# Performance work log

Measured on AMD Instinct MI355X. Metric: run time of the kernel, lower is better.

The kernel has to match this reference:

```python
import jax, jax.numpy as jnp
import numpy as np

POOL = 7                     # cfg.POOLING_SIZE
PRE = 2 * POOL               # pre_pool_size (max_pool=True path)
LEVEL_HW = (256, 128, 64, 32)  # square H=W of P2..P5 for a 1024x1024 image


def setup_inputs() -> dict:
    key = jax.random.key(0)
    ks = jax.random.split(key, 8)
    C = 256
    feats = {f"p{i + 2}": jax.random.normal(ks[i], (1, C, s, s), dtype=jnp.float32)
             for i, s in enumerate(LEVEL_HW)}
    N = 1000
    IMG = 1024.0
    x1 = jax.random.uniform(ks[4], (N,), minval=0.0, maxval=IMG - 33.0)
    y1 = jax.random.uniform(ks[5], (N,), minval=0.0, maxval=IMG - 33.0)
    w = jax.random.uniform(ks[6], (N,), minval=32.0, maxval=512.0)
    h = jax.random.uniform(ks[7], (N,), minval=32.0, maxval=512.0)
    x2 = jnp.minimum(x1 + w, IMG - 1.0)
    y2 = jnp.minimum(y1 + h, IMG - 1.0)
    rois = jnp.stack([jnp.zeros((N,), jnp.float32), x1, y1, x2, y2], axis=1)
    inp = dict(feats)
    inp["rois"] = rois
    return inp


def _crop_pool_fpn(p2, p3, p4, p5, rois):
    """Faithful vectorized version of Network._crop_pool_layer_fpn (max_pool=True).

    Per-ROI FPN level select, affine-grid + bilinear grid_sample
    (align_corners=True semantics, zeros padding), then 2x2 max pool.
    """
    levels = (p2, p3, p4, p5)
    C = p2.shape[1]
    Hm = p2.shape[2]  # largest (P2) map; all levels padded up to this
    # Pad every level into one [L, Hm, Wm, C] array (NHWC for clean gathers).
    feats = jnp.stack([
        jnp.pad(jnp.transpose(f[0], (1, 2, 0)),
                ((0, Hm - f.shape[2]), (0, Hm - f.shape[3]), (0, 0)))
        for f in levels])

    x1, y1, x2, y2 = rois[:, 1], rois[:, 2], rois[:, 3], rois[:, 4]
    w = jnp.where(x2 - x1 <= 0, 1e-14, x2 - x1)
    h = jnp.where(y2 - y1 <= 0, 1e-14, y2 - y1)
    kf = 4.0 + jnp.log2(jnp.sqrt(w * h) / 224.0)   # k0 + log2(sqrt(wh)/224)
    kf = jnp.clip(kf, 2.0, 5.0)                     # clamp BEFORE round (as in source)
    k = jnp.round(kf)
    scale = 2.0 ** k
    lvl = k.astype(jnp.int32) - 2                   # [N] in [0,4)
    x1s, y1s, x2s, y2s = x1 / scale, y1 / scale, x2 / scale, y2 / scale

    # affine_grid(theta) + align_corners=True grid_sample collapses to direct
    # pixel coords: px = (x1+x2)/2 + t*(x2-x1)/2, t = linspace(-1, 1, PRE).
    t = jnp.linspace(-1.0, 1.0, PRE)
    px = (x1s + x2s)[:, None] * 0.5 + t[None, :] * ((x2s - x1s)[:, None] * 0.5)  # [N,PRE]
    py = (y1s + y2s)[:, None] * 0.5 + t[None, :] * ((y2s - y1s)[:, None] * 0.5)
    PX = jnp.broadcast_to(px[:, None, :], (px.shape[0], PRE, PRE))  # [N,PRE,PRE]
    PY = jnp.broadcast_to(py[:, :, None], (py.shape[0], PRE, PRE))

    HWl = jnp.asarray(LEVEL_HW, jnp.float32)[lvl][:, None, None]  # per-ROI level size (square)
    x0 = jnp.floor(PX)
    y0 = jnp.floor(PY)
    dx = PX - x0
    dy = PY - y0

    def gather(yi, xi):
        inb = ((xi >= 0) & (xi < HWl) & (yi >= 0) & (yi < HWl)).astype(feats.dtype)
        yc = jnp.clip(yi, 0, Hm - 1).astype(jnp.int32)
        xc = jnp.clip(xi, 0, Hm - 1).astype(jnp.int32)
        v = feats[lvl[:, None, None], yc, xc]      # [N,PRE,PRE,C]
        return v * inb[..., None]                   # zeros padding

    out = (gather(y0, x0) * ((1 - dy) * (1 - dx))[..., None]
           + gather(y0, x0 + 1) * ((1 - dy) * dx)[..., None]
           + gather(y0 + 1, x0) * (dy * (1 - dx))[..., None]
           + gather(y0 + 1, x0 + 1) * (dy * dx)[..., None])  # [N,PRE,PRE,C]

    crops = jnp.transpose(out, (0, 3, 1, 2))        # [N,C,PRE,PRE]
    N = crops.shape[0]
    crops = crops.reshape(N, C, POOL, 2, POOL, 2).max(axis=(3, 5))  # 2x2 max pool
    return crops                                     # [N,C,POOL,POOL]


def reference(p2, p3, p4, p5, rois):
    return _crop_pool_fpn(p2, p3, p4, p5, rois)
```

## Files before the change

kernel.cpp:

```cpp
#include <hip/hip_runtime.h>
#include <math.h>

#define C_CH 256
#define PRE 14
#define NPOOL 7
#define PIX (NPOOL * NPOOL)
#define OUT_PER_ROI (C_CH * PIX)
#define HALF_C 128
#define HALF_OUT (HALF_C * PIX)
#define SROW 132

#define OFF_P2 0
#define OFF_P3 16777216u
#define OFF_P4 20971520u
#define OFF_P5 22020096u
#define WS_ELEMS 22282240u

#define RB 528

static __device__ __forceinline__ unsigned short f2bf(float f) {
    unsigned int u = __float_as_uint(f);
    unsigned int r = (u + 0x7FFFu + ((u >> 16) & 1u)) >> 16;
    return (unsigned short)r;
}
static __device__ __forceinline__ float bf2f(unsigned short b) {
    return __uint_as_float(((unsigned int)b) << 16);
}

__global__ __launch_bounds__(256) void transpose_all_k(
    const float* __restrict__ p2, const float* __restrict__ p3,
    const float* __restrict__ p4, const float* __restrict__ p5,
    unsigned short* __restrict__ ws) {
    __shared__ unsigned char lds[128 * RB];

    int b = blockIdx.x;
    const float* __restrict__ src;
    int HW2; unsigned int off;
    if (b < 512)      { src = p2; HW2 = 65536; off = OFF_P2; }
    else if (b < 640) { src = p3; HW2 = 16384; off = OFF_P3; b -= 512; }
    else if (b < 672) { src = p4; HW2 = 4096;  off = OFF_P4; b -= 640; }
    else              { src = p5; HW2 = 1024;  off = OFF_P5; b -= 672; }
    const int hw0 = b << 7;

    const int t   = threadIdx.x;
    const int hwq = t & 31;
    const int cg  = t >> 5;

    const int key = (hwq & 7) << 4;

    #pragma unroll
    for (int s = 0; s < 8; ++s) {
        const int c0 = (cg << 2) + (s << 5);
        const float* g = src + (size_t)c0 * HW2 + hw0 + (hwq << 2);
        const float4 a0 = *(const float4*)(g);
        const float4 a1 = *(const float4*)(g + HW2);
        const float4 a2 = *(const float4*)(g + 2 * (size_t)HW2);
        const float4 a3 = *(const float4*)(g + 3 * (size_t)HW2);
        const int cb = (c0 << 1) ^ key;
        unsigned char* base = &lds[(hwq << 2) * RB + cb];
        ushort4 w;
        w.x = f2bf(a0.x); w.y = f2bf(a1.x); w.z = f2bf(a2.x); w.w = f2bf(a3.x);
        *(ushort4*)(base) = w;
        w.x = f2bf(a0.y); w.y = f2bf(a1.y); w.z = f2bf(a2.y); w.w = f2bf(a3.y);
        *(ushort4*)(base + RB) = w;
        w.x = f2bf(a0.z); w.y = f2bf(a1.z); w.z = f2bf(a2.z); w.w = f2bf(a3.z);
        *(ushort4*)(base + 2 * RB) = w;
        w.x = f2bf(a0.w); w.y = f2bf(a1.w); w.z = f2bf(a2.w); w.w = f2bf(a3.w);
        *(ushort4*)(base + 3 * RB) = w;
    }
    __syncthreads();

    char* __restrict__ dstb = (char*)(ws + off + ((size_t)hw0 << 8));
    const int chunk = t & 31;
    const int hwl   = t >> 5;
    #pragma unroll
    for (int p = 0; p < 16; ++p) {
        const int hw = (p << 3) + hwl;
        const int k2 = ((hw >> 2) & 7) << 4;
        const uint4 v = *(const uint4*)&lds[hw * RB + ((chunk << 4) ^ k2)];
        *(uint4*)(dstb + hw * 512 + (chunk << 4)) = v;
    }
}

template <bool HWC>
__global__ __launch_bounds__(256, 6) void roi_align_k(
    const float* __restrict__ p2, const float* __restrict__ p3,
    const float* __restrict__ p4, const float* __restrict__ p5,
    const unsigned short* __restrict__ ws, const float* __restrict__ rois,
    float* __restrict__ out) {

    __shared__ float sxw0[PRE], sxw1[PRE], syw0[PRE], syw1[PRE];
    __shared__ int   sxc0[PRE], sxc1[PRE], syc0[PRE], syc1[PRE];
    __shared__ float sout[PIX * SROW];

    const int n   = blockIdx.x;
    const int ch0 = blockIdx.y << 7;
    const float x1 = rois[n * 5 + 1];
    const float y1 = rois[n * 5 + 2];
    const float x2 = rois[n * 5 + 3];
    const float y2 = rois[n * 5 + 4];

    float w = x2 - x1; w = (w <= 0.f) ? 1e-14f : w;
    float h = y2 - y1; h = (h <= 0.f) ? 1e-14f : h;
    float kf = 4.f + log2f(sqrtf(w * h) * (1.f / 224.f));
    kf = fminf(fmaxf(kf, 2.f), 5.f);
    const float kr = rintf(kf);
    const int   lvl = (int)kr - 2;
    const float scale = exp2f(kr);
    const int   HW = 256 >> lvl;

    const int t = threadIdx.x;

    if (t < 2 * PRE) {
        const bool isx = t < PRE;
        const int  j = isx ? t : t - PRE;
        const float a1 = isx ? x1 : y1;
        const float a2 = isx ? x2 : y2;
        const float a1s = a1 / scale, a2s = a2 / scale;
        const float cen  = (a1s + a2s) * 0.5f;
        const float half = (a2s - a1s) * 0.5f;
        const float tt = -1.f + (2.f / 13.f) * (float)j;
        const float p  = cen + tt * half;
        const float p0 = floorf(p);
        const float d  = p - p0;
        const float HWf = (float)HW;
        const float m0 = (p0 >= 0.f && p0 < HWf) ? 1.f : 0.f;
        const float m1 = (p0 + 1.f >= 0.f && p0 + 1.f < HWf) ? 1.f : 0.f;
        const int c0i = min(max((int)p0, 0), HW - 1);
        const int c1i = min(max((int)p0 + 1, 0), HW - 1);
        if (isx) { sxw0[j] = (1.f - d) * m0; sxw1[j] = d * m1; sxc0[j] = c0i; sxc1[j] = c1i; }
        else     { syw0[j] = (1.f - d) * m0; syw1[j] = d * m1; syc0[j] = c0i; syc1[j] = c1i; }
    }
    __syncthreads();

    const int g     = t & 31;
    const int ph    = t >> 5;
    const int cbase = ch0 + (g << 2);

    const unsigned short* __restrict__ fb = nullptr;
    const float* __restrict__ fbF = nullptr;
    if (HWC) {
        const unsigned int off = (lvl == 0) ? OFF_P2 : (lvl == 1) ? OFF_P3 : (lvl == 2) ? OFF_P4 : OFF_P5;
        fb = ws + off + cbase;
    } else {
        fbF = (lvl == 0) ? p2 : (lvl == 1) ? p3 : (lvl == 2) ? p4 : p5;
    }
    const int HW2 = HW * HW;

    for (int p = ph; p < PIX; p += 8) {
        const int oy = p / 7;
        const int ox = p - oy * 7;
        float4 m = make_float4(-3.4e38f, -3.4e38f, -3.4e38f, -3.4e38f);
        #pragma unroll
        for (int sy = 0; sy < 2; ++sy) {
            const int i = oy * 2 + sy;
            const float wy0 = syw0[i], wy1 = syw1[i];
            const int   yc0 = syc0[i], yc1 = syc1[i];
            #pragma unroll
            for (int sx = 0; sx < 2; ++sx) {
                const int j = ox * 2 + sx;
                const float wx0 = sxw0[j], wx1 = sxw1[j];
                const int   xc0 = sxc0[j], xc1 = sxc1[j];
                float4 v;
                if (HWC) {
                    const ushort4 a00 = *(const ushort4*)(fb + ((yc0 * HW + xc0) << 8));
                    const ushort4 a01 = *(const ushort4*)(fb + ((yc0 * HW + xc1) << 8));
                    const ushort4 a10 = *(const ushort4*)(fb + ((yc1 * HW + xc0) << 8));
                    const ushort4 a11 = *(const ushort4*)(fb + ((yc1 * HW + xc1) << 8));
                    v.x = wy0 * (wx0 * bf2f(a00.x) + wx1 * bf2f(a01.x)) + wy1 * (wx0 * bf2f(a10.x) + wx1 * bf2f(a11.x));
                    v.y = wy0 * (wx0 * bf2f(a00.y) + wx1 * bf2f(a01.y)) + wy1 * (wx0 * bf2f(a10.y) + wx1 * bf2f(a11.y));
                    v.z = wy0 * (wx0 * bf2f(a00.z) + wx1 * bf2f(a01.z)) + wy1 * (wx0 * bf2f(a10.z) + wx1 * bf2f(a11.z));
                    v.w = wy0 * (wx0 * bf2f(a00.w) + wx1 * bf2f(a01.w)) + wy1 * (wx0 * bf2f(a10.w) + wx1 * bf2f(a11.w));
                } else {
                    float vv[4];
                    #pragma unroll
                    for (int k = 0; k < 4; ++k) {
                        const size_t cb = (size_t)(cbase + k) * HW2;
                        const float a00 = fbF[cb + yc0 * HW + xc0];
                        const float a01 = fbF[cb + yc0 * HW + xc1];
                        const float a10 = fbF[cb + yc1 * HW + xc0];
                        const float a11 = fbF[cb + yc1 * HW + xc1];
                        vv[k] = wy0 * (wx0 * a00 + wx1 * a01) + wy1 * (wx0 * a10 + wx1 * a11);
                    }
                    v.x = vv[0]; v.y = vv[1]; v.z = vv[2]; v.w = vv[3];
                }
                m.x = fmaxf(m.x, v.x);
                m.y = fmaxf(m.y, v.y);
                m.z = fmaxf(m.z, v.z);
                m.w = fmaxf(m.w, v.w);
            }
        }
        *(float4*)&sout[p * SROW + (g << 2)] = m;
    }
    __syncthreads();

    const size_t ob = (size_t)n * OUT_PER_ROI + (size_t)ch0 * PIX;
    for (int o = t; o < HALF_OUT; o += 256) {
        const int c  = o / PIX;
        const int pp = o - c * PIX;
        out[ob + o] = sout[pp * SROW + c];
    }
}

extern "C" void kernel_launch(void* const* d_in, const int* in_sizes, int n_in,
                              void* d_out, int out_size, void* d_ws, size_t ws_size,
                              hipStream_t stream) {
    const float* p2   = (const float*)d_in[0];
    const float* p3   = (const float*)d_in[1];
    const float* p4   = (const float*)d_in[2];
    const float* p5   = (const float*)d_in[3];
    const float* rois = (const float*)d_in[4];
    float* out = (float*)d_out;
    const int N = in_sizes[4] / 5;

    const size_t need = (size_t)WS_ELEMS * sizeof(unsigned short);
    if (ws_size >= need) {
        unsigned short* ws = (unsigned short*)d_ws;
        transpose_all_k<<<680, 256, 0, stream>>>(p2, p3, p4, p5, ws);
        roi_align_k<true><<<dim3(N, 2), 256, 0, stream>>>(p2, p3, p4, p5, ws, rois, out);
    } else {
        roi_align_k<false><<<dim3(N, 2), 256, 0, stream>>>(p2, p3, p4, p5, nullptr, rois, out);
    }
}
```

Measured before the change: 56.25 us.

## Sort ROIs by level and position for locality, add nontemporal loads/stores

Adds an extra block to the transpose kernel that computes a key per ROI (FPN level, then the scaled y/x corner) and bitonic-sorts the ROIs in LDS, writing a permutation to the workspace. The ROI-align kernel then processes ROIs in that order so that neighbouring blocks gather overlapping feature regions and get more cache reuse. It also uses nontemporal loads for the one-pass feature reads and nontemporal stores for the output, and precomputes the four bilinear weights for an FMA chain. In exchange, the sort adds a serial block that may lengthen the transpose kernel's tail, and the fast path now requires N <= 1024.

```diff
diff --git a/kernel.cpp b/kernel.cpp
--- a/kernel.cpp
+++ b/kernel.cpp
@@ -17,6 +17,9 @@
 #define WS_ELEMS 22282240u
 
 #define RB 528
+#define NTRANS 680
+
+typedef float f4v __attribute__((ext_vector_type(4)));
 
 static __device__ __forceinline__ unsigned short f2bf(float f) {
     unsigned int u = __float_as_uint(f);
@@ -30,8 +33,49 @@
 __global__ __launch_bounds__(256) void transpose_all_k(
     const float* __restrict__ p2, const float* __restrict__ p3,
     const float* __restrict__ p4, const float* __restrict__ p5,
-    unsigned short* __restrict__ ws) {
+    unsigned short* __restrict__ ws, const float* __restrict__ rois,
+    unsigned* __restrict__ perm, int N) {
     __shared__ unsigned char lds[128 * RB];
+
+    if (blockIdx.x == NTRANS) {
+        unsigned long long* kv = (unsigned long long*)lds;
+        const int t = threadIdx.x;
+        for (int i = t; i < 1024; i += 256) {
+            unsigned key = 0xFFFFFFFFu;
+            if (i < N) {
+                const float x1 = rois[i * 5 + 1];
+                const float y1 = rois[i * 5 + 2];
+                const float x2 = rois[i * 5 + 3];
+                const float y2 = rois[i * 5 + 4];
+                float w = x2 - x1; w = (w <= 0.f) ? 1e-14f : w;
+                float h = y2 - y1; h = (h <= 0.f) ? 1e-14f : h;
+                float kf = 4.f + log2f(sqrtf(w * h) * (1.f / 224.f));
+                kf = fminf(fmaxf(kf, 2.f), 5.f);
+                const float kr = rintf(kf);
+                const int lvl = (int)kr - 2;
+                const float inv = exp2f(-kr);
+                const int yi = (int)(y1 * inv);
+                const int xi = (int)(x1 * inv);
+                key = ((unsigned)lvl << 26) | ((unsigned)yi << 13) | (unsigned)xi;
+            }
+            kv[i] = ((unsigned long long)key << 32) | (unsigned)i;
+        }
+        __syncthreads();
+        for (int k = 2; k <= 1024; k <<= 1) {
+            for (int j = k >> 1; j > 0; j >>= 1) {
+                for (int i = t; i < 512; i += 256) {
+                    const int e = (i << 1) - (i & (j - 1));
+                    const int f = e | j;
+                    const bool up = ((e & k) == 0);
+                    const unsigned long long A = kv[e], B = kv[f];
+                    if ((A > B) == up) { kv[e] = B; kv[f] = A; }
+                }
+                __syncthreads();
+            }
+        }
+        for (int i = t; i < N; i += 256) perm[i] = (unsigned)kv[i];
+        return;
+    }
 
     int b = blockIdx.x;
     const float* __restrict__ src;
@@ -52,10 +96,10 @@
     for (int s = 0; s < 8; ++s) {
         const int c0 = (cg << 2) + (s << 5);
         const float* g = src + (size_t)c0 * HW2 + hw0 + (hwq << 2);
-        const float4 a0 = *(const float4*)(g);
-        const float4 a1 = *(const float4*)(g + HW2);
-        const float4 a2 = *(const float4*)(g + 2 * (size_t)HW2);
-        const float4 a3 = *(const float4*)(g + 3 * (size_t)HW2);
+        const f4v a0 = __builtin_nontemporal_load((const f4v*)(g));
+        const f4v a1 = __builtin_nontemporal_load((const f4v*)(g + HW2));
+        const f4v a2 = __builtin_nontemporal_load((const f4v*)(g + 2 * (size_t)HW2));
+        const f4v a3 = __builtin_nontemporal_load((const f4v*)(g + 3 * (size_t)HW2));
         const int cb = (c0 << 1) ^ key;
         unsigned char* base = &lds[(hwq << 2) * RB + cb];
         ushort4 w;
@@ -87,13 +131,13 @@
     const float* __restrict__ p2, const float* __restrict__ p3,
     const float* __restrict__ p4, const float* __restrict__ p5,
     const unsigned short* __restrict__ ws, const float* __restrict__ rois,
-    float* __restrict__ out) {
+    const unsigned* __restrict__ perm, float* __restrict__ out) {
 
     __shared__ float sxw0[PRE], sxw1[PRE], syw0[PRE], syw1[PRE];
     __shared__ int   sxc0[PRE], sxc1[PRE], syc0[PRE], syc1[PRE];
     __shared__ float sout[PIX * SROW];
 
-    const int n   = blockIdx.x;
+    const int n   = HWC ? (int)perm[blockIdx.x] : (int)blockIdx.x;
     const int ch0 = blockIdx.y << 7;
     const float x1 = rois[n * 5 + 1];
     const float y1 = rois[n * 5 + 2];
@@ -161,16 +205,18 @@
                 const int j = ox * 2 + sx;
                 const float wx0 = sxw0[j], wx1 = sxw1[j];
                 const int   xc0 = sxc0[j], xc1 = sxc1[j];
+                const float w00 = wy0 * wx0, w01 = wy0 * wx1;
+                const float w10 = wy1 * wx0, w11 = wy1 * wx1;
                 float4 v;
                 if (HWC) {
                     const ushort4 a00 = *(const ushort4*)(fb + ((yc0 * HW + xc0) << 8));
                     const ushort4 a01 = *(const ushort4*)(fb + ((yc0 * HW + xc1) << 8));
                     const ushort4 a10 = *(const ushort4*)(fb + ((yc1 * HW + xc0) << 8));
                     const ushort4 a11 = *(const ushort4*)(fb + ((yc1 * HW + xc1) << 8));
-                    v.x = wy0 * (wx0 * bf2f(a00.x) + wx1 * bf2f(a01.x)) + wy1 * (wx0 * bf2f(a10.x) + wx1 * bf2f(a11.x));
-                    v.y = wy0 * (wx0 * bf2f(a00.y) + wx1 * bf2f(a01.y)) + wy1 * (wx0 * bf2f(a10.y) + wx1 * bf2f(a11.y));
-                    v.z = wy0 * (wx0 * bf2f(a00.z) + wx1 * bf2f(a01.z)) + wy1 * (wx0 * bf2f(a10.z) + wx1 * bf2f(a11.z));
-                    v.w = wy0 * (wx0 * bf2f(a00.w) + wx1 * bf2f(a01.w)) + wy1 * (wx0 * bf2f(a10.w) + wx1 * bf2f(a11.w));
+                    v.x = fmaf(bf2f(a00.x), w00, fmaf(bf2f(a01.x), w01, fmaf(bf2f(a10.x), w10, bf2f(a11.x) * w11)));
+                    v.y = fmaf(bf2f(a00.y), w00, fmaf(bf2f(a01.y), w01, fmaf(bf2f(a10.y), w10, bf2f(a11.y) * w11)));
+                    v.z = fmaf(bf2f(a00.z), w00, fmaf(bf2f(a01.z), w01, fmaf(bf2f(a10.z), w10, bf2f(a11.z) * w11)));
+                    v.w = fmaf(bf2f(a00.w), w00, fmaf(bf2f(a01.w), w01, fmaf(bf2f(a10.w), w10, bf2f(a11.w) * w11)));
                 } else {
                     float vv[4];
                     #pragma unroll
@@ -180,7 +226,7 @@
                         const float a01 = fbF[cb + yc0 * HW + xc1];
                         const float a10 = fbF[cb + yc1 * HW + xc0];
                         const float a11 = fbF[cb + yc1 * HW + xc1];
-                        vv[k] = wy0 * (wx0 * a00 + wx1 * a01) + wy1 * (wx0 * a10 + wx1 * a11);
+                        vv[k] = fmaf(a00, w00, fmaf(a01, w01, fmaf(a10, w10, a11 * w11)));
                     }
                     v.x = vv[0]; v.y = vv[1]; v.z = vv[2]; v.w = vv[3];
                 }
@@ -198,7 +244,7 @@
     for (int o = t; o < HALF_OUT; o += 256) {
         const int c  = o / PIX;
         const int pp = o - c * PIX;
-        out[ob + o] = sout[pp * SROW + c];
+        __builtin_nontemporal_store(sout[pp * SROW + c], &out[ob + o]);
     }
 }
 
@@ -213,12 +259,13 @@
     float* out = (float*)d_out;
     const int N = in_sizes[4] / 5;
 
-    const size_t need = (size_t)WS_ELEMS * sizeof(unsigned short);
-    if (ws_size >= need) {
+    const size_t need = (size_t)WS_ELEMS * sizeof(unsigned short) + 4096;
+    if (ws_size >= need && N <= 1024) {
         unsigned short* ws = (unsigned short*)d_ws;
-        transpose_all_k<<<680, 256, 0, stream>>>(p2, p3, p4, p5, ws);
-        roi_align_k<true><<<dim3(N, 2), 256, 0, stream>>>(p2, p3, p4, p5, ws, rois, out);
+        unsigned* perm = (unsigned*)((char*)d_ws + (size_t)WS_ELEMS * sizeof(unsigned short));
+        transpose_all_k<<<NTRANS + 1, 256, 0, stream>>>(p2, p3, p4, p5, ws, rois, perm, N);
+        roi_align_k<true><<<dim3(N, 2), 256, 0, stream>>>(p2, p3, p4, p5, ws, rois, perm, out);
     } else {
-        roi_align_k<false><<<dim3(N, 2), 256, 0, stream>>>(p2, p3, p4, p5, nullptr, rois, out);
-    }
-}
+        roi_align_k<false><<<dim3(N, 2), 256, 0, stream>>>(p2, p3, p4, p5, nullptr, rois, nullptr, out);
+    }
+}
```

Measured after the change: 77.44 us. 1.38x slower.
